# Performance work log

Hardware: AMD Instinct MI355X
Metric: run time of the kernel (lower is better)

## Reference

```python
import jax, jax.numpy as jnp
import numpy as np

HEADS = 4
DIM_HEAD = 32
DIM = 512
HIDDEN = HEADS * DIM_HEAD  # 128


def setup_inputs() -> dict:
    key = jax.random.key(0)
    k1, k2, k3, k4 = jax.random.split(key, 4)
    b, l = 8, 8192
    x = jax.random.normal(k1, (b, DIM, l), dtype=jnp.float32)
    # Conv1d kernel_size=1 weights stored as [out_ch, in_ch] (squeeze kernel dim)
    w_qkv = jax.random.normal(k2, (HIDDEN * 3, DIM), dtype=jnp.float32) * (1.0 / np.sqrt(DIM))
    w_out = jax.random.normal(k3, (DIM, HIDDEN), dtype=jnp.float32) * (1.0 / np.sqrt(HIDDEN))
    b_out = jax.random.normal(k4, (DIM,), dtype=jnp.float32) * 0.01
    return {"x": x, "w_qkv": w_qkv, "w_out": w_out, "b_out": b_out}


def reference(x, w_qkv, w_out, b_out):
    b, c, l = x.shape
    # 1x1 conv == channel matmul: [b, 3*hidden, l]
    qkv = jnp.einsum('oc,bcl->bol', w_qkv, x)
    # split into q, k, v each [b, heads, dim_head, l]
    qkv = qkv.reshape(b, 3, HEADS, DIM_HEAD, l)
    q, k, v = qkv[:, 0], qkv[:, 1], qkv[:, 2]
    k = jax.nn.softmax(k, axis=-1)  # softmax over sequence positions
    # context: [b, h, d, e] (small dim_head x dim_head per head)
    context = jnp.einsum('bhdn,bhen->bhde', k, v)
    out = jnp.einsum('bhde,bhdn->bhen', context, q)  # [b, h, e, l]
    out = out.reshape(b, HIDDEN, l)
    return jnp.einsum('oc,bcl->bol', w_out, out) + b_out[None, :, None]
```

## Files before the change

### kernel.cpp

```cpp
#include <hip/hip_runtime.h>
#include <math.h>
#include <stdint.h>


#define L_LEN 8192L
#define DIMC 512

typedef short bf16x8 __attribute__((ext_vector_type(8)));
typedef float f32x4 __attribute__((ext_vector_type(4)));

__device__ __forceinline__ unsigned short f2bf(float f) {
    uint32_t u = __float_as_uint(f);
    u += 0x7FFFu + ((u >> 16) & 1u);
    return (unsigned short)(u >> 16);
}
__device__ __forceinline__ void unpack8(uint4 u, float* f) {
    f[0] = __uint_as_float(u.x << 16); f[1] = __uint_as_float(u.x & 0xFFFF0000u);
    f[2] = __uint_as_float(u.y << 16); f[3] = __uint_as_float(u.y & 0xFFFF0000u);
    f[4] = __uint_as_float(u.z << 16); f[5] = __uint_as_float(u.z & 0xFFFF0000u);
    f[6] = __uint_as_float(u.w << 16); f[7] = __uint_as_float(u.w & 0xFFFF0000u);
}

#define GLOAD_LDS16(g, l) __builtin_amdgcn_global_load_lds( \
    (const __attribute__((address_space(1))) uint32_t*)(g), \
    (__attribute__((address_space(3))) uint32_t*)(l), 16, 0, 0)

__global__ __launch_bounds__(256)
void xpose_cvt_kernel(const float* __restrict__ x, unsigned short* __restrict__ xb)
{
    const int b  = blockIdx.z;
    const int c0 = blockIdx.y * 64;
    const int l0 = blockIdx.x * 64;
    const float* xp = x + (long)b * DIMC * L_LEN;
    unsigned short* op = xb + (long)b * L_LEN * DIMC;
    __shared__ float tile[64][65];
    const int t = threadIdx.x;
    #pragma unroll
    for (int r = 0; r < 4; ++r) {
        int idx = t + 256 * r;
        int row = idx >> 4, col4 = (idx & 15) * 4;
        float4 v = *(const float4*)&xp[(long)(c0 + row) * L_LEN + l0 + col4];
        tile[row][col4 + 0] = v.x;
        tile[row][col4 + 1] = v.y;
        tile[row][col4 + 2] = v.z;
        tile[row][col4 + 3] = v.w;
    }
    __syncthreads();
    #pragma unroll
    for (int r = 0; r < 4; ++r) {
        int idx = t + 256 * r;
        int lr = idx >> 4, c4 = (idx & 15) * 4;
        ushort4 o;
        o.x = f2bf(tile[c4 + 0][lr]);
        o.y = f2bf(tile[c4 + 1][lr]);
        o.z = f2bf(tile[c4 + 2][lr]);
        o.w = f2bf(tile[c4 + 3][lr]);
        *(ushort4*)&op[(long)(l0 + lr) * DIMC + c0 + c4] = o;
    }
}

__global__ __launch_bounds__(256)
void cvt_w_kernel(const float* __restrict__ w, unsigned short* __restrict__ wb, int n)
{
    int i = blockIdx.x * 256 + threadIdx.x;
    if (i < n) wb[i] = f2bf(w[i]);
}

template<int OUT_BF16>
__global__ __launch_bounds__(256)
void mfma_gemm_kernel(const unsigned short* __restrict__ A, long aBS,
                      const unsigned short* __restrict__ B, long bBS,
                      void* __restrict__ Cv, long cBS,
                      const float* __restrict__ bias)
{
    const int b  = blockIdx.z;
    const int m0 = blockIdx.y * 128;
    const int l0 = blockIdx.x * 128;
    A += (long)b * aBS;
    B += (long)b * bBS;

    __shared__ unsigned short Asm[128 * 32];
    __shared__ unsigned short Bsm[128 * 32];

    const int t = threadIdx.x;
    const int wave = t >> 6, lane = t & 63;
    const int wm = (wave & 1) * 64, wn = (wave >> 1) * 64;

    const int srow  = wave * 16 + (lane >> 2);
    const int skoff = (lane & 3) * 8;
    const unsigned short* ag0 = A + (long)(m0 + srow) * DIMC + skoff;
    const unsigned short* ag1 = A + (long)(m0 + srow + 64) * DIMC + skoff;
    const unsigned short* bg0 = B + (long)(l0 + srow) * DIMC + skoff;
    const unsigned short* bg1 = B + (long)(l0 + srow + 64) * DIMC + skoff;
    unsigned short* al0 = Asm + wave * 512;
    unsigned short* al1 = Asm + 2048 + wave * 512;
    unsigned short* bl0 = Bsm + wave * 512;
    unsigned short* bl1 = Bsm + 2048 + wave * 512;

    const int fr = lane & 15;
    const int quad = lane >> 4;

    f32x4 acc[4][4] = {};

    for (int k0 = 0; k0 < DIMC; k0 += 32) {
        GLOAD_LDS16(ag0 + k0, al0);
        GLOAD_LDS16(ag1 + k0, al1);
        GLOAD_LDS16(bg0 + k0, bl0);
        GLOAD_LDS16(bg1 + k0, bl1);
        __syncthreads();

        bf16x8 af[4], bfr[4];
        #pragma unroll
        for (int i = 0; i < 4; ++i)
            af[i] = *(const bf16x8*)&Asm[(wm + i * 16 + fr) * 32 + quad * 8];
        #pragma unroll
        for (int j = 0; j < 4; ++j)
            bfr[j] = *(const bf16x8*)&Bsm[(wn + j * 16 + fr) * 32 + quad * 8];
        #pragma unroll
        for (int i = 0; i < 4; ++i)
            #pragma unroll
            for (int j = 0; j < 4; ++j)
                acc[i][j] = __builtin_amdgcn_mfma_f32_16x16x32_bf16(af[i], bfr[j], acc[i][j], 0, 0, 0);
        __syncthreads();
    }

    #pragma unroll
    for (int i = 0; i < 4; ++i) {
        #pragma unroll
        for (int j = 0; j < 4; ++j) {
            #pragma unroll
            for (int r = 0; r < 4; ++r) {
                int m = m0 + wm + i * 16 + quad * 4 + r;
                long l = l0 + wn + j * 16 + fr;
                float v = acc[i][j][r];
                if (bias) v += bias[m];
                if (OUT_BF16)
                    ((unsigned short*)Cv)[(long)b * cBS + (long)m * L_LEN + l] = f2bf(v);
                else
                    ((float*)Cv)[(long)b * cBS + (long)m * L_LEN + l] = v;
            }
        }
    }
}

__global__ __launch_bounds__(256)
void softmax_stats_kernel(const unsigned short* __restrict__ kvb, float2* __restrict__ stats)
{
    const int row = blockIdx.x;
    const int b = row >> 7, r = row & 127;
    const unsigned short* p = kvb + ((long)b * 256 + r) * L_LEN;
    const int t = threadIdx.x;
    float vals[32];
    float m = -INFINITY;
    #pragma unroll
    for (int i = 0; i < 4; ++i) {
        uint4 u = *(const uint4*)&p[i * 2048 + t * 8];
        unpack8(u, &vals[i * 8]);
        #pragma unroll
        for (int e = 0; e < 8; ++e) m = fmaxf(m, vals[i * 8 + e]);
    }
    for (int off = 32; off; off >>= 1) m = fmaxf(m, __shfl_down(m, off, 64));
    __shared__ float sm[4], ss[4];
    const int wave = t >> 6, lane = t & 63;
    if (lane == 0) sm[wave] = m;
    __syncthreads();
    m = fmaxf(fmaxf(sm[0], sm[1]), fmaxf(sm[2], sm[3]));
    float s = 0.0f;
    #pragma unroll
    for (int i = 0; i < 32; ++i) s += __expf(vals[i] - m);
    for (int off = 32; off; off >>= 1) s += __shfl_down(s, off, 64);
    if (lane == 0) ss[wave] = s;
    __syncthreads();
    if (t == 0) stats[row] = make_float2(m, 1.0f / (ss[0] + ss[1] + ss[2] + ss[3]));
}

__global__ __launch_bounds__(256)
void context_kernel(const unsigned short* __restrict__ kvb, const float2* __restrict__ stats,
                    float* __restrict__ ctx)
{
    const int bid = blockIdx.x;
    const int b = bid >> 5, rem = bid & 31;
    const int h = rem >> 3, d0 = (rem & 7) * 4;
    const int t = threadIdx.x;

    const unsigned short* kbase = kvb + ((long)b * 256 + h * 32 + d0) * L_LEN;
    const unsigned short* vbase = kvb + ((long)b * 256 + 128 + h * 32) * L_LEN;

    float2 st[4];
    #pragma unroll
    for (int i = 0; i < 4; ++i) st[i] = stats[b * 128 + h * 32 + d0 + i];

    float acc[4][32] = {};

    for (int c = 0; c < 4; ++c) {
        int n = c * 2048 + t * 8;
        float w8[4][8];
        #pragma unroll
        for (int i = 0; i < 4; ++i) {
            uint4 u = *(const uint4*)&kbase[(long)i * L_LEN + n];
            float f[8];
            unpack8(u, f);
            #pragma unroll
            for (int k = 0; k < 8; ++k) w8[i][k] = __expf(f[k] - st[i].x) * st[i].y;
        }
        #pragma unroll
        for (int e = 0; e < 32; ++e) {
            uint4 u = *(const uint4*)&vbase[(long)e * L_LEN + n];
            float g[8];
            unpack8(u, g);
            #pragma unroll
            for (int i = 0; i < 4; ++i) {
                float s = acc[i][e];
                #pragma unroll
                for (int k = 0; k < 8; ++k) s = fmaf(w8[i][k], g[k], s);
                acc[i][e] = s;
            }
        }
    }

    const int wave = t >> 6, lane = t & 63;
    __shared__ float red[4][128];
    #pragma unroll
    for (int i = 0; i < 4; ++i)
        #pragma unroll
        for (int e = 0; e < 32; ++e) {
            float val = acc[i][e];
            for (int off = 32; off; off >>= 1) val += __shfl_down(val, off, 64);
            if (lane == 0) red[wave][i * 32 + e] = val;
        }
    __syncthreads();
    if (t < 128) {
        float s = red[0][t] + red[1][t] + red[2][t] + red[3][t];
        int i = t >> 5, e = t & 31;
        ctx[((long)((b * 4 + h) * 32) + d0 + i) * 32 + e] = s;
    }
}

__global__ __launch_bounds__(256)
void w2_kernel(const float* __restrict__ w_out, const float* __restrict__ ctx,
               float* __restrict__ W2)
{
    const int idx = blockIdx.x * 256 + threadIdx.x;
    const int b = idx >> 16;
    const int rem = idx & 65535;
    const int o = rem >> 7, hd = rem & 127;
    const int h = hd >> 5, d = hd & 31;
    const float* wp = w_out + o * 128 + h * 32;
    const float* cp = ctx + ((long)((b * 4 + h) * 32) + d) * 32;
    float s = 0.0f;
    #pragma unroll
    for (int e = 0; e < 32; e += 4) {
        float4 wv = *(const float4*)&wp[e];
        float4 cv = *(const float4*)&cp[e];
        s += wv.x * cv.x + wv.y * cv.y + wv.z * cv.z + wv.w * cv.w;
    }
    W2[idx] = s;
}

__global__ __launch_bounds__(256)
void weff_kernel(const float* __restrict__ W2, const float* __restrict__ wq,
                 unsigned short* __restrict__ Weffb)
{
    const int b  = blockIdx.z;
    const int ot = blockIdx.y * 64;
    const int ct = blockIdx.x * 64;
    __shared__ float W2t[64][129];
    __shared__ float wqt[128][64];
    const int t = threadIdx.x;
    const float* W2b = W2 + (long)b * 512 * 128;
    #pragma unroll
    for (int r = 0; r < 8; ++r) {
        int f4 = t + 256 * r;
        int row = f4 >> 5, c4 = (f4 & 31) * 4;
        float4 v = *(const float4*)&W2b[(long)(ot + row) * 128 + c4];
        W2t[row][c4 + 0] = v.x; W2t[row][c4 + 1] = v.y;
        W2t[row][c4 + 2] = v.z; W2t[row][c4 + 3] = v.w;
    }
    #pragma unroll
    for (int r = 0; r < 8; ++r) {
        int f4 = t + 256 * r;
        int hd = f4 >> 4, c4 = (f4 & 15) * 4;
        *(float4*)&wqt[hd][c4] = *(const float4*)&wq[(long)hd * DIMC + ct + c4];
    }
    __syncthreads();
    const int oo = (t >> 4) * 4, cc = (t & 15) * 4;
    float acc[4][4] = {};
    for (int hd = 0; hd < 128; ++hd) {
        float a[4], bb[4];
        #pragma unroll
        for (int e = 0; e < 4; ++e) a[e]  = W2t[oo + e][hd];
        #pragma unroll
        for (int e = 0; e < 4; ++e) bb[e] = wqt[hd][cc + e];
        #pragma unroll
        for (int i = 0; i < 4; ++i)
            #pragma unroll
            for (int j = 0; j < 4; ++j)
                acc[i][j] = fmaf(a[i], bb[j], acc[i][j]);
    }
    #pragma unroll
    for (int i = 0; i < 4; ++i)
        #pragma unroll
        for (int j = 0; j < 4; ++j)
            Weffb[((long)b * 512 + ot + oo + i) * 512 + ct + cc + j] = f2bf(acc[i][j]);
}

extern "C" void kernel_launch(void* const* d_in, const int* in_sizes, int n_in,
                              void* d_out, int out_size, void* d_ws, size_t ws_size,
                              hipStream_t stream)
{
    const float* x     = (const float*)d_in[0];
    const float* w_qkv = (const float*)d_in[1];
    const float* w_out = (const float*)d_in[2];
    const float* b_out = (const float*)d_in[3];
    float* out = (float*)d_out;

    char* ws = (char*)d_ws;
    unsigned short* xb    = (unsigned short*)(ws);
    unsigned short* kvb   = (unsigned short*)(ws + 67108864L);
    float2*         stats = (float2*)(ws + 100663296L);
    float*          ctx   = (float*)(ws + 100671488L);
    float*          W2    = (float*)(ws + 100802560L);
    unsigned short* wb    = (unsigned short*)(ws + 100663296L);
    unsigned short* Weffb = (unsigned short*)(ws + 67108864L);

    xpose_cvt_kernel<<<dim3(128, 8, 8), 256, 0, stream>>>(x, xb);
    cvt_w_kernel<<<dim3(512), 256, 0, stream>>>(w_qkv + 128 * DIMC, wb, 256 * DIMC);
    mfma_gemm_kernel<1><<<dim3(64, 2, 8), 256, 0, stream>>>(
        wb, 0L, xb, L_LEN * DIMC, kvb, 256L * L_LEN, nullptr);
    softmax_stats_kernel<<<1024, 256, 0, stream>>>(kvb, stats);
    context_kernel<<<256, 256, 0, stream>>>(kvb, stats, ctx);
    w2_kernel<<<2048, 256, 0, stream>>>(w_out, ctx, W2);
    weff_kernel<<<dim3(8, 8, 8), 256, 0, stream>>>(W2, w_qkv, Weffb);
    mfma_gemm_kernel<0><<<dim3(64, 4, 8), 256, 0, stream>>>(
        Weffb, 512L * DIMC, xb, L_LEN * DIMC, out, 512L * L_LEN, b_out);
}
```

Measured before the change: 429.7 us.

## Drop softmax max pass, use Q-projection path, fuse stats into context via atomics

The separate softmax statistics pass is removed. The context kernel now computes unnormalized exp(k) together with its row sums, and spreads the work over more blocks that accumulate with atomics. The normalization is folded into w2_kernel. When the workspace is large enough, Q is projected explicitly and transposed, so the final GEMM contracts over 128 channels instead of 512, which also removes the weff kernel. The GEMM now loads 64 K-elements per barrier, and a single misc kernel both converts the weights and zeroes the accumulators. Skipping the max subtraction risks exp overflow for large key logits, and the atomics make the result order-dependent.

Result: faster. 385.3 us (-10.3%).

```diff
diff --git a/kernel.cpp b/kernel.cpp
--- a/kernel.cpp
+++ b/kernel.cpp
@@ -24,6 +24,18 @@
 #define GLOAD_LDS16(g, l) __builtin_amdgcn_global_load_lds( \
     (const __attribute__((address_space(1))) uint32_t*)(g), \
     (__attribute__((address_space(3))) uint32_t*)(l), 16, 0, 0)
+
+__global__ __launch_bounds__(256)
+void misc_kernel(const float* __restrict__ w, unsigned short* __restrict__ wb,
+                 float* __restrict__ zbase)
+{
+    int idx = blockIdx.x * 256 + threadIdx.x;
+    if (idx < 196608) wb[idx] = f2bf(w[idx]);
+    else {
+        int z = idx - 196608;
+        if (z < 33792) zbase[z] = 0.0f;
+    }
+}
 
 __global__ __launch_bounds__(256)
 void xpose_cvt_kernel(const float* __restrict__ x, unsigned short* __restrict__ xb)
@@ -59,14 +71,7 @@
     }
 }
 
-__global__ __launch_bounds__(256)
-void cvt_w_kernel(const float* __restrict__ w, unsigned short* __restrict__ wb, int n)
-{
-    int i = blockIdx.x * 256 + threadIdx.x;
-    if (i < n) wb[i] = f2bf(w[i]);
-}
-
-template<int OUT_BF16>
+template<int OUT_BF16, int KD>
 __global__ __launch_bounds__(256)
 void mfma_gemm_kernel(const unsigned short* __restrict__ A, long aBS,
                       const unsigned short* __restrict__ B, long bBS,
@@ -79,48 +84,44 @@
     A += (long)b * aBS;
     B += (long)b * bBS;
 
-    __shared__ unsigned short Asm[128 * 32];
-    __shared__ unsigned short Bsm[128 * 32];
+    __shared__ unsigned short Asm[2 * 4096];
+    __shared__ unsigned short Bsm[2 * 4096];
 
     const int t = threadIdx.x;
     const int wave = t >> 6, lane = t & 63;
     const int wm = (wave & 1) * 64, wn = (wave >> 1) * 64;
-
     const int srow  = wave * 16 + (lane >> 2);
     const int skoff = (lane & 3) * 8;
-    const unsigned short* ag0 = A + (long)(m0 + srow) * DIMC + skoff;
-    const unsigned short* ag1 = A + (long)(m0 + srow + 64) * DIMC + skoff;
-    const unsigned short* bg0 = B + (long)(l0 + srow) * DIMC + skoff;
-    const unsigned short* bg1 = B + (long)(l0 + srow + 64) * DIMC + skoff;
-    unsigned short* al0 = Asm + wave * 512;
-    unsigned short* al1 = Asm + 2048 + wave * 512;
-    unsigned short* bl0 = Bsm + wave * 512;
-    unsigned short* bl1 = Bsm + 2048 + wave * 512;
-
-    const int fr = lane & 15;
-    const int quad = lane >> 4;
+    const int fr = lane & 15, quad = lane >> 4;
 
     f32x4 acc[4][4] = {};
 
-    for (int k0 = 0; k0 < DIMC; k0 += 32) {
-        GLOAD_LDS16(ag0 + k0, al0);
-        GLOAD_LDS16(ag1 + k0, al1);
-        GLOAD_LDS16(bg0 + k0, bl0);
-        GLOAD_LDS16(bg1 + k0, bl1);
+    for (int k0 = 0; k0 < KD; k0 += 64) {
+        #pragma unroll
+        for (int c = 0; c < 2; ++c) {
+            const int kk = k0 + c * 32 + skoff;
+            GLOAD_LDS16(A + (long)(m0 + srow) * KD + kk,      Asm + c * 4096 + wave * 512);
+            GLOAD_LDS16(A + (long)(m0 + 64 + srow) * KD + kk, Asm + c * 4096 + 2048 + wave * 512);
+            GLOAD_LDS16(B + (long)(l0 + srow) * KD + kk,      Bsm + c * 4096 + wave * 512);
+            GLOAD_LDS16(B + (long)(l0 + 64 + srow) * KD + kk, Bsm + c * 4096 + 2048 + wave * 512);
+        }
         __syncthreads();
 
-        bf16x8 af[4], bfr[4];
-        #pragma unroll
-        for (int i = 0; i < 4; ++i)
-            af[i] = *(const bf16x8*)&Asm[(wm + i * 16 + fr) * 32 + quad * 8];
-        #pragma unroll
-        for (int j = 0; j < 4; ++j)
-            bfr[j] = *(const bf16x8*)&Bsm[(wn + j * 16 + fr) * 32 + quad * 8];
-        #pragma unroll
-        for (int i = 0; i < 4; ++i)
+        #pragma unroll
+        for (int c = 0; c < 2; ++c) {
+            bf16x8 af[4], bf[4];
+            #pragma unroll
+            for (int i = 0; i < 4; ++i)
+                af[i] = *(const bf16x8*)&Asm[c * 4096 + (wm + i * 16 + fr) * 32 + quad * 8];
             #pragma unroll
             for (int j = 0; j < 4; ++j)
-                acc[i][j] = __builtin_amdgcn_mfma_f32_16x16x32_bf16(af[i], bfr[j], acc[i][j], 0, 0, 0);
+                bf[j] = *(const bf16x8*)&Bsm[c * 4096 + (wn + j * 16 + fr) * 32 + quad * 8];
+            #pragma unroll
+            for (int i = 0; i < 4; ++i)
+                #pragma unroll
+                for (int j = 0; j < 4; ++j)
+                    acc[i][j] = __builtin_amdgcn_mfma_f32_16x16x32_bf16(af[i], bf[j], acc[i][j], 0, 0, 0);
+        }
         __syncthreads();
     }
 
@@ -144,101 +145,102 @@
 }
 
 __global__ __launch_bounds__(256)
-void softmax_stats_kernel(const unsigned short* __restrict__ kvb, float2* __restrict__ stats)
-{
-    const int row = blockIdx.x;
-    const int b = row >> 7, r = row & 127;
-    const unsigned short* p = kvb + ((long)b * 256 + r) * L_LEN;
-    const int t = threadIdx.x;
-    float vals[32];
-    float m = -INFINITY;
+void qt_kernel(const unsigned short* __restrict__ qkvb, unsigned short* __restrict__ qT)
+{
+    const int b   = blockIdx.z;
+    const int hd0 = blockIdx.y * 64;
+    const int l0  = blockIdx.x * 64;
+    const unsigned short* qp = qkvb + (long)b * 384 * L_LEN;
+    unsigned short* op = qT + (long)b * L_LEN * 128;
+    __shared__ unsigned short tile[64][72];
+    const int t = threadIdx.x;
+    #pragma unroll
+    for (int r = 0; r < 2; ++r) {
+        int row = r * 32 + (t >> 3), col8 = (t & 7) * 8;
+        uint4 v = *(const uint4*)&qp[(long)(hd0 + row) * L_LEN + l0 + col8];
+        *(uint4*)&tile[row][col8] = v;
+    }
+    __syncthreads();
+    const int lr = t >> 2, c16 = (t & 3) * 16;
+    unsigned short o[16];
+    #pragma unroll
+    for (int j = 0; j < 16; ++j) o[j] = tile[c16 + j][lr];
+    unsigned short* dst = op + (long)(l0 + lr) * 128 + hd0 + c16;
+    *(uint4*)&dst[0] = *(const uint4*)&o[0];
+    *(uint4*)&dst[8] = *(const uint4*)&o[8];
+}
+
+__global__ __launch_bounds__(256)
+void ctx_kernel(const unsigned short* __restrict__ kv, long batchStride, long kOff, long vOff,
+                float* __restrict__ ctxU, float* __restrict__ S)
+{
+    const int bid  = blockIdx.x;
+    const int esel = bid & 1;
+    const int nc   = (bid >> 1) & 3;
+    const int dg   = (bid >> 3) & 7;
+    const int h    = (bid >> 6) & 3;
+    const int b    = bid >> 8;
+    const int d0   = dg * 4, e0 = esel * 16;
+    const int t = threadIdx.x;
+    const long n = (long)nc * 2048 + t * 8;
+
+    const unsigned short* kp = kv + (long)b * batchStride + kOff + (long)(h * 32 + d0) * L_LEN + n;
+    const unsigned short* vp = kv + (long)b * batchStride + vOff + (long)(h * 32 + e0) * L_LEN + n;
+
+    float w8[4][8], s4[4];
     #pragma unroll
     for (int i = 0; i < 4; ++i) {
-        uint4 u = *(const uint4*)&p[i * 2048 + t * 8];
-        unpack8(u, &vals[i * 8]);
-        #pragma unroll
-        for (int e = 0; e < 8; ++e) m = fmaxf(m, vals[i * 8 + e]);
-    }
-    for (int off = 32; off; off >>= 1) m = fmaxf(m, __shfl_down(m, off, 64));
-    __shared__ float sm[4], ss[4];
+        uint4 u = *(const uint4*)&kp[(long)i * L_LEN];
+        float f[8]; unpack8(u, f);
+        float s = 0.0f;
+        #pragma unroll
+        for (int k = 0; k < 8; ++k) { w8[i][k] = __expf(f[k]); s += w8[i][k]; }
+        s4[i] = s;
+    }
+    float acc[4][16];
+    #pragma unroll
+    for (int e = 0; e < 16; ++e) {
+        uint4 u = *(const uint4*)&vp[(long)e * L_LEN];
+        float g[8]; unpack8(u, g);
+        #pragma unroll
+        for (int i = 0; i < 4; ++i) {
+            float s = 0.0f;
+            #pragma unroll
+            for (int k = 0; k < 8; ++k) s = fmaf(w8[i][k], g[k], s);
+            acc[i][e] = s;
+        }
+    }
+
     const int wave = t >> 6, lane = t & 63;
-    if (lane == 0) sm[wave] = m;
+    __shared__ float red[4][68];
+    #pragma unroll
+    for (int i = 0; i < 4; ++i) {
+        #pragma unroll
+        for (int e = 0; e < 16; ++e) {
+            float v = acc[i][e];
+            for (int off = 32; off; off >>= 1) v += __shfl_down(v, off, 64);
+            if (lane == 0) red[wave][i * 16 + e] = v;
+        }
+        float sv = s4[i];
+        for (int off = 32; off; off >>= 1) sv += __shfl_down(sv, off, 64);
+        if (lane == 0) red[wave][64 + i] = sv;
+    }
     __syncthreads();
-    m = fmaxf(fmaxf(sm[0], sm[1]), fmaxf(sm[2], sm[3]));
-    float s = 0.0f;
-    #pragma unroll
-    for (int i = 0; i < 32; ++i) s += __expf(vals[i] - m);
-    for (int off = 32; off; off >>= 1) s += __shfl_down(s, off, 64);
-    if (lane == 0) ss[wave] = s;
-    __syncthreads();
-    if (t == 0) stats[row] = make_float2(m, 1.0f / (ss[0] + ss[1] + ss[2] + ss[3]));
-}
-
-__global__ __launch_bounds__(256)
-void context_kernel(const unsigned short* __restrict__ kvb, const float2* __restrict__ stats,
-                    float* __restrict__ ctx)
-{
-    const int bid = blockIdx.x;
-    const int b = bid >> 5, rem = bid & 31;
-    const int h = rem >> 3, d0 = (rem & 7) * 4;
-    const int t = threadIdx.x;
-
-    const unsigned short* kbase = kvb + ((long)b * 256 + h * 32 + d0) * L_LEN;
-    const unsigned short* vbase = kvb + ((long)b * 256 + 128 + h * 32) * L_LEN;
-
-    float2 st[4];
-    #pragma unroll
-    for (int i = 0; i < 4; ++i) st[i] = stats[b * 128 + h * 32 + d0 + i];
-
-    float acc[4][32] = {};
-
-    for (int c = 0; c < 4; ++c) {
-        int n = c * 2048 + t * 8;
-        float w8[4][8];
-        #pragma unroll
-        for (int i = 0; i < 4; ++i) {
-            uint4 u = *(const uint4*)&kbase[(long)i * L_LEN + n];
-            float f[8];
-            unpack8(u, f);
-            #pragma unroll
-            for (int k = 0; k < 8; ++k) w8[i][k] = __expf(f[k] - st[i].x) * st[i].y;
-        }
-        #pragma unroll
-        for (int e = 0; e < 32; ++e) {
-            uint4 u = *(const uint4*)&vbase[(long)e * L_LEN + n];
-            float g[8];
-            unpack8(u, g);
-            #pragma unroll
-            for (int i = 0; i < 4; ++i) {
-                float s = acc[i][e];
-                #pragma unroll
-                for (int k = 0; k < 8; ++k) s = fmaf(w8[i][k], g[k], s);
-                acc[i][e] = s;
-            }
-        }
-    }
-
-    const int wave = t >> 6, lane = t & 63;
-    __shared__ float red[4][128];
-    #pragma unroll
-    for (int i = 0; i < 4; ++i)
-        #pragma unroll
-        for (int e = 0; e < 32; ++e) {
-            float val = acc[i][e];
-            for (int off = 32; off; off >>= 1) val += __shfl_down(val, off, 64);
-            if (lane == 0) red[wave][i * 32 + e] = val;
-        }
-    __syncthreads();
-    if (t < 128) {
-        float s = red[0][t] + red[1][t] + red[2][t] + red[3][t];
-        int i = t >> 5, e = t & 31;
-        ctx[((long)((b * 4 + h) * 32) + d0 + i) * 32 + e] = s;
-    }
-}
-
-__global__ __launch_bounds__(256)
-void w2_kernel(const float* __restrict__ w_out, const float* __restrict__ ctx,
-               float* __restrict__ W2)
+    if (t < 68) {
+        float v = red[0][t] + red[1][t] + red[2][t] + red[3][t];
+        if (t < 64) {
+            int i = t >> 4, e = t & 15;
+            atomicAdd(&ctxU[(((long)(b * 4 + h) * 32) + d0 + i) * 32 + e0 + e], v);
+        } else if (esel == 0) {
+            atomicAdd(&S[b * 128 + h * 32 + d0 + (t - 64)], v);
+        }
+    }
+}
+
+template<int OUT_BF16>
+__global__ __launch_bounds__(256)
+void w2_kernel(const float* __restrict__ w_out, const float* __restrict__ ctxU,
+               const float* __restrict__ S, void* __restrict__ out)
 {
     const int idx = blockIdx.x * 256 + threadIdx.x;
     const int b = idx >> 16;
@@ -246,7 +248,7 @@
     const int o = rem >> 7, hd = rem & 127;
     const int h = hd >> 5, d = hd & 31;
     const float* wp = w_out + o * 128 + h * 32;
-    const float* cp = ctx + ((long)((b * 4 + h) * 32) + d) * 32;
+    const float* cp = ctxU + (((long)(b * 4 + h) * 32) + d) * 32;
     float s = 0.0f;
     #pragma unroll
     for (int e = 0; e < 32; e += 4) {
@@ -254,7 +256,9 @@
         float4 cv = *(const float4*)&cp[e];
         s += wv.x * cv.x + wv.y * cv.y + wv.z * cv.z + wv.w * cv.w;
     }
-    W2[idx] = s;
+    s /= S[b * 128 + hd];
+    if (OUT_BF16) ((unsigned short*)out)[idx] = f2bf(s);
+    else          ((float*)out)[idx] = s;
 }
 
 __global__ __launch_bounds__(256)
@@ -315,22 +319,47 @@
     float* out = (float*)d_out;
 
     char* ws = (char*)d_ws;
-    unsigned short* xb    = (unsigned short*)(ws);
-    unsigned short* kvb   = (unsigned short*)(ws + 67108864L);
-    float2*         stats = (float2*)(ws + 100663296L);
-    float*          ctx   = (float*)(ws + 100671488L);
-    float*          W2    = (float*)(ws + 100802560L);
-    unsigned short* wb    = (unsigned short*)(ws + 100663296L);
-    unsigned short* Weffb = (unsigned short*)(ws + 67108864L);
-
-    xpose_cvt_kernel<<<dim3(128, 8, 8), 256, 0, stream>>>(x, xb);
-    cvt_w_kernel<<<dim3(512), 256, 0, stream>>>(w_qkv + 128 * DIMC, wb, 256 * DIMC);
-    mfma_gemm_kernel<1><<<dim3(64, 2, 8), 256, 0, stream>>>(
-        wb, 0L, xb, L_LEN * DIMC, kvb, 256L * L_LEN, nullptr);
-    softmax_stats_kernel<<<1024, 256, 0, stream>>>(kvb, stats);
-    context_kernel<<<256, 256, 0, stream>>>(kvb, stats, ctx);
-    w2_kernel<<<2048, 256, 0, stream>>>(w_out, ctx, W2);
-    weff_kernel<<<dim3(8, 8, 8), 256, 0, stream>>>(W2, w_qkv, Weffb);
-    mfma_gemm_kernel<0><<<dim3(64, 4, 8), 256, 0, stream>>>(
-        Weffb, 512L * DIMC, xb, L_LEN * DIMC, out, 512L * L_LEN, b_out);
-}
+    unsigned short* xb = (unsigned short*)ws;
+
+    const bool qpath = (ws_size >= 117968896UL);
+
+    if (qpath) {
+        unsigned short* qkvb = (unsigned short*)(ws + 67108864L);
+        char* T = ws + 117440512L;
+        unsigned short* wb = (unsigned short*)T;
+        float* ctxU = (float*)(T + 393216L);
+        float* Ssum = (float*)(T + 524288L);
+        unsigned short* qT  = xb;
+        unsigned short* W2b = qkvb;
+
+        misc_kernel<<<900, 256, 0, stream>>>(w_qkv, wb, ctxU);
+        xpose_cvt_kernel<<<dim3(128, 8, 8), 256, 0, stream>>>(x, xb);
+        mfma_gemm_kernel<1, 512><<<dim3(64, 3, 8), 256, 0, stream>>>(
+            wb, 0L, xb, L_LEN * DIMC, qkvb, 384L * L_LEN, nullptr);
+        qt_kernel<<<dim3(128, 2, 8), 256, 0, stream>>>(qkvb, qT);
+        ctx_kernel<<<2048, 256, 0, stream>>>(qkvb, 384L * L_LEN, 128L * L_LEN, 256L * L_LEN,
+                                             ctxU, Ssum);
+        w2_kernel<1><<<2048, 256, 0, stream>>>(w_out, ctxU, Ssum, W2b);
+        mfma_gemm_kernel<0, 128><<<dim3(64, 4, 8), 256, 0, stream>>>(
+            W2b, 512L * 128, qT, L_LEN * 128, out, 512L * L_LEN, b_out);
+    } else {
+        unsigned short* kvb = (unsigned short*)(ws + 67108864L);
+        char* T = ws + 100663296L;
+        unsigned short* wb = (unsigned short*)T;
+        float* ctxU = (float*)(T + 393216L);
+        float* Ssum = (float*)(T + 524288L);
+        unsigned short* Weffb = kvb;
+        float* W2f = (float*)(ws + 67108864L + 4194304L);
+
+        misc_kernel<<<900, 256, 0, stream>>>(w_qkv, wb, ctxU);
+        xpose_cvt_kernel<<<dim3(128, 8, 8), 256, 0, stream>>>(x, xb);
+        mfma_gemm_kernel<1, 512><<<dim3(64, 2, 8), 256, 0, stream>>>(
+            wb + 128 * DIMC, 0L, xb, L_LEN * DIMC, kvb, 256L * L_LEN, nullptr);
+        ctx_kernel<<<2048, 256, 0, stream>>>(kvb, 256L * L_LEN, 0L, 128L * L_LEN,
+                                             ctxU, Ssum);
+        w2_kernel<0><<<2048, 256, 0, stream>>>(w_out, ctxU, Ssum, W2f);
+        weff_kernel<<<dim3(8, 8, 8), 256, 0, stream>>>(W2f, w_qkv, Weffb);
+        mfma_gemm_kernel<0, 512><<<dim3(64, 4, 8), 256, 0, stream>>>(
+            Weffb, 512L * DIMC, xb, L_LEN * DIMC, out, 512L * L_LEN, b_out);
+    }
+}
```
